# Kernel optimization log

Hardware: AMD Instinct MI355X
Metric: run time of the kernel (lower is better)

## Reference

```python
import jax, jax.numpy as jnp
import numpy as np

H = 8  # num_heads
EPS = 1e-5

def _layernorm(x, g, b):
    mu = jnp.mean(x, axis=-1, keepdims=True)
    var = jnp.var(x, axis=-1, keepdims=True)
    return (x - mu) * jax.lax.rsqrt(var + EPS) * g + b

def setup_inputs() -> dict:
    key = jax.random.key(0)
    ks = jax.random.split(key, 16)
    B, S, D, F = 1, 4096, 512, 2048
    s = 1.0 / np.sqrt(D)
    inp = {
        'x': jax.random.normal(ks[0], (B, S, D), jnp.float32),
        'mask': jax.random.randint(ks[1], (S, S), 0, 2, jnp.int32),
        'wq': jax.random.normal(ks[2], (D, D), jnp.float32) * s,
        'bq': jnp.zeros((D,), jnp.float32),
        'wk': jax.random.normal(ks[3], (D, D), jnp.float32) * s,
        'bk': jnp.zeros((D,), jnp.float32),
        'wv': jax.random.normal(ks[4], (D, D), jnp.float32) * s,
        'bv': jnp.zeros((D,), jnp.float32),
        'wo': jax.random.normal(ks[5], (D, D), jnp.float32) * s,
        'bo': jnp.zeros((D,), jnp.float32),
        'w1': jax.random.normal(ks[6], (D, F), jnp.float32) * s,
        'b1': jnp.zeros((F,), jnp.float32),
        'w2': jax.random.normal(ks[7], (F, D), jnp.float32) * (1.0 / np.sqrt(F)),
        'b2': jnp.zeros((D,), jnp.float32),
        'g1': jnp.ones((D,), jnp.float32),
        'be1': jnp.zeros((D,), jnp.float32),
        'g2': jnp.ones((D,), jnp.float32),
        'be2': jnp.zeros((D,), jnp.float32),
    }
    return inp

def reference(x, mask, wq, bq, wk, bk, wv, bv, wo, bo, w1, b1, w2, b2, g1, be1, g2, be2):
    B, S, D = x.shape
    Dh = D // H

    def split(t):  # (B,S,D) -> (B,H,S,Dh)
        return t.reshape(B, S, H, Dh).transpose(0, 2, 1, 3)

    q = split(x @ wq + bq)
    k = split(x @ wk + bk)
    v = split(x @ wv + bv)

    # naive attention: full (B,H,S,S) scores, NO 1/sqrt(Dh) scaling (faithful to source)
    scores = jnp.einsum('bhsd,bhtd->bhst', q, k)
    scores = jnp.where(mask == 0, jnp.float32(-1e9), scores)
    attn = jax.nn.softmax(scores, axis=-1)
    out = jnp.einsum('bhst,bhtd->bhsd', attn, v)
    out = out.transpose(0, 2, 1, 3).reshape(B, S, D) @ wo + bo

    x = _layernorm(x + out, g1, be1)  # dropout is identity at inference
    ff = jax.nn.relu(x @ w1 + b1) @ w2 + b2
    x = _layernorm(x + ff, g2, be2)
    return x
```

## Files before the change

### kernel.cpp

```cpp
#include <hip/hip_runtime.h>

typedef unsigned short u16;
typedef unsigned int u32;
typedef unsigned long long u64;
typedef __attribute__((ext_vector_type(4))) float f32x4;
typedef __attribute__((ext_vector_type(8))) short bf16x8;
typedef __attribute__((ext_vector_type(4))) u16 u16x4;
typedef __attribute__((ext_vector_type(2))) u32 u32x2;

#define DEV __device__ __forceinline__

DEV u16 f2bf(float f) {
  union { float f; u32 u; } c; c.f = f;
  u32 u = c.u;
  u += 0x7fffu + ((u >> 16) & 1u);
  return (u16)(u >> 16);
}
DEV u32 fbits(float f) { union { float f; u32 u; } c; c.f = f; return c.u; }
DEV u32 packbits(u32 a, u32 b) {
  return __builtin_amdgcn_perm(b, a, 0x07060302u);
}

DEV void gload_lds16(const void* g, void* l) {
  __builtin_amdgcn_global_load_lds(
      (const __attribute__((address_space(1))) u32*)(u64)g,
      (__attribute__((address_space(3))) u32*)(u32)(u64)l,
      16, 0, 0);
}

struct PrepW { const float* w; u16* th; int R, C, gxmask, gxshift; };
struct PrepArgs {
  const float* x; u16* xh;
  const int* mask; unsigned long long* mbits;
  PrepW pw[6];
};

__global__ __launch_bounds__(256) void prep(PrepArgs a) {
  __shared__ float t[32][33];
  int b = blockIdx.x, tid = threadIdx.x;
  if (b < 2048) {
    int i = (b * 256 + tid) * 4;
    f32x4 v = *(const f32x4*)(a.x + i);
    u16x4 h;
#pragma unroll
    for (int j = 0; j < 4; ++j) h[j] = f2bf(v[j]);
    *(u16x4*)(a.xh + i) = h;
    return;
  }
  b -= 2048;
  if (b < 3072) {
    int wi, base;
    if (b < 1024) { wi = b >> 8; base = b & 255; }
    else if (b < 2048) { wi = 4; base = b - 1024; }
    else { wi = 5; base = b - 2048; }
    PrepW p = a.pw[wi];
    int c0 = (base & p.gxmask) * 32, r0 = (base >> p.gxshift) * 32;
    int tx = tid & 31, ty = tid >> 5;
#pragma unroll
    for (int i = 0; i < 4; ++i)
      t[ty + 8 * i][tx] = p.w[(size_t)(r0 + ty + 8 * i) * p.C + c0 + tx];
    __syncthreads();
#pragma unroll
    for (int i = 0; i < 4; ++i)
      p.th[(size_t)(c0 + ty + 8 * i) * p.R + r0 + tx] = f2bf(t[tx][ty + 8 * i]);
    return;
  }
  b -= 3072;
  size_t i = (size_t)b * 256 + tid;
  unsigned long long bb = __ballot(a.mask[i] != 0);
  if ((tid & 63) == 0) a.mbits[i >> 6] = bb;
}

struct QkvArgs {
  const u16* Ah;
  const u16* Bh[3];
  const float* bias[3];
  u16 *Qh, *Kh, *Vt;
};

__global__ __launch_bounds__(256) void gemm_qkv(QkvArgs a) {
  const int K = 512;
  const float L2E = 1.44269504088896340736f;
  const int z = blockIdx.z;
  const u16* __restrict__ Bh = a.Bh[z];
  const float* __restrict__ bias = a.bias[z];
  const int bn = blockIdx.x * 128, bm = blockIdx.y * 128;
  const int tid = threadIdx.x;
  const int wave = tid >> 6, lane = tid & 63;
  const int l16 = lane & 15, quad = lane >> 4;
  const int wm = (wave >> 1) * 64, wn = (wave & 1) * 64;

  __shared__ u16 sA[2][128 * 32];
  __shared__ u16 sB[2][128 * 32];

  const int srow = wave * 32 + (lane >> 2);
  const int scol = (lane & 3) * 8;
  const u16* srcA0 = a.Ah + (size_t)(bm + srow) * K + scol;
  const u16* srcB0 = Bh + (size_t)(bn + srow) * K + scol;
  const size_t half_off = (size_t)16 * K;

  auto prefetchG = [&](int kt, int buf) {
    u16* dA = sA[buf] + wave * 1024;
    u16* dB = sB[buf] + wave * 1024;
    gload_lds16(srcA0 + kt, dA);
    gload_lds16(srcA0 + half_off + kt, dA + 512);
    gload_lds16(srcB0 + kt, dB);
    gload_lds16(srcB0 + half_off + kt, dB + 512);
  };

  f32x4 acc[4][4] = {};
  prefetchG(0, 0);

  for (int i = 0; i < 16; ++i) {
    __syncthreads();
    if (i + 1 < 16) prefetchG((i + 1) << 5, (i + 1) & 1);
    const u16* bufA = sA[i & 1];
    const u16* bufB = sB[i & 1];

    bf16x8 a_h[4], b_h[4];
#pragma unroll
    for (int mt = 0; mt < 4; ++mt)
      a_h[mt] = *(const bf16x8*)(bufA + (wm + mt * 16 + l16) * 32 + quad * 8);
#pragma unroll
    for (int nt = 0; nt < 4; ++nt)
      b_h[nt] = *(const bf16x8*)(bufB + (wn + nt * 16 + l16) * 32 + quad * 8);
#pragma unroll
    for (int mt = 0; mt < 4; ++mt)
#pragma unroll
      for (int nt = 0; nt < 4; ++nt)
        acc[mt][nt] = __builtin_amdgcn_mfma_f32_16x16x32_bf16(a_h[mt], b_h[nt], acc[mt][nt], 0, 0, 0);
  }

  if (z == 2) {
#pragma unroll
    for (int nt = 0; nt < 4; ++nt) {
      int col = bn + wn + nt * 16 + l16;
      float bv = bias[col];
#pragma unroll
      for (int mt = 0; mt < 4; ++mt) {
        int row0 = bm + wm + mt * 16 + quad * 4;
        u16x4 o;
#pragma unroll
        for (int r = 0; r < 4; ++r) o[r] = f2bf(acc[mt][nt][r] + bv);
        *(u16x4*)(a.Vt + (size_t)col * 4096 + row0) = o;
      }
    }
  } else {
    u16* __restrict__ C = (z == 0) ? a.Qh : a.Kh;
    float scale = (z == 0) ? L2E : 1.f;
#pragma unroll
    for (int mt = 0; mt < 4; ++mt)
#pragma unroll
      for (int nt = 0; nt < 4; ++nt) {
        int col = bn + wn + nt * 16 + l16;
        float bv = bias[col];
#pragma unroll
        for (int r = 0; r < 4; ++r) {
          int row = bm + wm + mt * 16 + quad * 4 + r;
          C[(size_t)row * 512 + col] = f2bf((acc[mt][nt][r] + bv) * scale);
        }
      }
  }
}

template <int RELU, int BF16OUT, int NSPLIT>
__global__ __launch_bounds__(256) void gemm_bt(const u16* __restrict__ Ah,
                                               const u16* __restrict__ Bh,
                                               const float* __restrict__ bias,
                                               float* __restrict__ Cf,
                                               float* __restrict__ Cf2,
                                               u16* __restrict__ Ch,
                                               int N, int K) {
  const int z = (NSPLIT > 1) ? blockIdx.z : 0;
  const int Ksub = K / NSPLIT;
  const int kbeg = z * Ksub;
  const int bn = blockIdx.x * 128, bm = blockIdx.y * 128;
  const int tid = threadIdx.x;
  const int wave = tid >> 6, lane = tid & 63;
  const int l16 = lane & 15, quad = lane >> 4;
  const int wm = (wave >> 1) * 64, wn = (wave & 1) * 64;

  __shared__ u16 sA[2][128 * 32];
  __shared__ u16 sB[2][128 * 32];

  const int srow = wave * 32 + (lane >> 2);
  const int scol = (lane & 3) * 8;
  const u16* srcA0 = Ah + (size_t)(bm + srow) * K + kbeg + scol;
  const u16* srcB0 = Bh + (size_t)(bn + srow) * K + kbeg + scol;
  const size_t half_off = (size_t)16 * K;

  auto prefetchG = [&](int kt, int buf) {
    u16* dA = sA[buf] + wave * 1024;
    u16* dB = sB[buf] + wave * 1024;
    gload_lds16(srcA0 + kt, dA);
    gload_lds16(srcA0 + half_off + kt, dA + 512);
    gload_lds16(srcB0 + kt, dB);
    gload_lds16(srcB0 + half_off + kt, dB + 512);
  };

  f32x4 acc[4][4] = {};
  prefetchG(0, 0);

  const int steps = Ksub >> 5;
  for (int i = 0; i < steps; ++i) {
    __syncthreads();
    if (i + 1 < steps) prefetchG((i + 1) << 5, (i + 1) & 1);
    const u16* bufA = sA[i & 1];
    const u16* bufB = sB[i & 1];

    bf16x8 a_h[4], b_h[4];
#pragma unroll
    for (int mt = 0; mt < 4; ++mt)
      a_h[mt] = *(const bf16x8*)(bufA + (wm + mt * 16 + l16) * 32 + quad * 8);
#pragma unroll
    for (int nt = 0; nt < 4; ++nt)
      b_h[nt] = *(const bf16x8*)(bufB + (wn + nt * 16 + l16) * 32 + quad * 8);
#pragma unroll
    for (int mt = 0; mt < 4; ++mt)
#pragma unroll
      for (int nt = 0; nt < 4; ++nt)
        acc[mt][nt] = __builtin_amdgcn_mfma_f32_16x16x32_bf16(a_h[mt], b_h[nt], acc[mt][nt], 0, 0, 0);
  }

  float* __restrict__ Co = (NSPLIT > 1 && z == 1) ? Cf2 : Cf;
#pragma unroll
  for (int mt = 0; mt < 4; ++mt)
#pragma unroll
    for (int nt = 0; nt < 4; ++nt) {
      int col = bn + wn + nt * 16 + l16;
      float bv = (bias && z == 0) ? bias[col] : 0.f;
#pragma unroll
      for (int r = 0; r < 4; ++r) {
        int row = bm + wm + mt * 16 + quad * 4 + r;
        float v = acc[mt][nt][r] + bv;
        if (RELU) v = fmaxf(v, 0.f);
        size_t oidx = (size_t)row * N + col;
        if (BF16OUT) Ch[oidx] = f2bf(v);
        else Co[oidx] = v;
      }
    }
}

struct AttnIO { float* O[4]; float* lp; };

__global__ __launch_bounds__(256) void attn(const u16* __restrict__ Qh,
                                            const u16* __restrict__ Kh,
                                            const u16* __restrict__ Vt,
                                            const u64* __restrict__ mb64,
                                            AttnIO io) {
  const int S = 4096, D = 512;
  const int h = blockIdx.x >> 2, chunk = blockIdx.x & 3;
  const int tid = threadIdx.x, wave = tid >> 6, lane = tid & 63;
  const int l16 = lane & 15, quad = lane >> 4;
  const int q0w = blockIdx.y * 128 + wave * 32;
  const int kbeg = chunk * 1024;
  const int sw = l16 & 7;

  __shared__ u16 sK[64 * 64];
  __shared__ u16 sV[2][80 * 64];
  __shared__ u16 sP[4][32 * 40];
  u16* myP = &sP[wave][0];

  if (tid < 32) ((u64*)(sV[tid >> 4] + 64 * 64))[tid & 15] = 0x3F803F803F803F80ULL;

  const int skey = lane >> 3;
  const int sch  = lane & 7;
  const u16* srcK = Kh + (size_t)(kbeg + wave * 8 + skey) * D + h * 64 + ((sch ^ skey) * 8);
  const u16* srcV = Vt + (size_t)(h * 64 + wave * 8 + skey) * S + kbeg + ((sch ^ skey) * 8);
  u16* dstK = sK + wave * 512;

  auto stageK = [&](int it) {
    const u16* p = srcK + (size_t)it * 64 * D;
    gload_lds16(p, dstK);
    gload_lds16(p + (size_t)32 * D, dstK + 32 * 64);
  };
  auto stageV = [&](int it) {
    const u16* p = srcV + it * 64;
    u16* d = sV[it & 1] + wave * 512;
    gload_lds16(p, d);
    gload_lds16(p + (size_t)32 * S, d + 32 * 64);
  };

  bf16x8 qf[2][2];
#pragma unroll
  for (int qt = 0; qt < 2; ++qt)
#pragma unroll
    for (int kd = 0; kd < 2; ++kd)
      qf[qt][kd] = *(const bf16x8*)(Qh + (size_t)(q0w + qt * 16 + l16) * D + h * 64 + kd * 32 + quad * 8);

  f32x4 accO[2][5] = {};
  const int wbase = kbeg >> 6;

  stageV(0);
  stageK(0);
  u64 wmCur[2];
#pragma unroll
  for (int qt = 0; qt < 2; ++qt)
    wmCur[qt] = mb64[(size_t)(q0w + qt * 16 + l16) * 64 + wbase];

  for (int it = 0; it < 16; ++it) {
    __syncthreads();
    if (it + 1 < 16) stageV(it + 1);
    u64 wmNext[2] = {0, 0};
    if (it + 1 < 16) {
#pragma unroll
      for (int qt = 0; qt < 2; ++qt)
        wmNext[qt] = mb64[(size_t)(q0w + qt * 16 + l16) * 64 + wbase + it + 1];
    }
    u32 wlo[2], whi[2];
#pragma unroll
    for (int qt = 0; qt < 2; ++qt) {
      wlo[qt] = (u32)(wmCur[qt] >> (quad * 4));
      whi[qt] = (u32)(wmCur[qt] >> (quad * 4 + 32));
    }

    f32x4 sc[4][2];
#pragma unroll
    for (int kt4 = 0; kt4 < 4; ++kt4) {
      const u16* arow = sK + (kt4 * 16 + l16) * 64;
      bf16x8 ka0 = *(const bf16x8*)(arow + ((quad ^ sw) * 8));
      bf16x8 ka1 = *(const bf16x8*)(arow + (((4 + quad) ^ sw) * 8));
#pragma unroll
      for (int qt = 0; qt < 2; ++qt) {
        f32x4 s = {};
        s = __builtin_amdgcn_mfma_f32_16x16x32_bf16(ka0, qf[qt][0], s, 0, 0, 0);
        s = __builtin_amdgcn_mfma_f32_16x16x32_bf16(ka1, qf[qt][1], s, 0, 0, 0);
        sc[kt4][qt] = s;
      }
    }
#pragma unroll
    for (int k2 = 0; k2 < 2; ++k2) {
#pragma unroll
      for (int qt = 0; qt < 2; ++qt) {
        u32 pb[4];
#pragma unroll
        for (int r = 0; r < 4; ++r) {
          u32 m = (u32)((int)(wlo[qt] << (31 - (k2 * 16 + r))) >> 31);
          pb[r] = fbits(__builtin_amdgcn_exp2f(sc[k2][qt][r])) & m;
        }
        u32x2 pk = {packbits(pb[0], pb[1]), packbits(pb[2], pb[3])};
        *(u32x2*)(myP + (qt * 16 + l16) * 40 + k2 * 16 + quad * 4) = pk;
      }
    }
    __syncthreads();
    if (it + 1 < 16) stageK(it + 1);
    const u16* bV = sV[it & 1];

    {
      bf16x8 pa[2];
#pragma unroll
      for (int qt = 0; qt < 2; ++qt)
        pa[qt] = *(const bf16x8*)(myP + (qt * 16 + l16) * 40 + quad * 8);
#pragma unroll
      for (int nt = 0; nt < 5; ++nt) {
        bf16x8 vf = *(const bf16x8*)(bV + (nt * 16 + l16) * 64 + ((quad ^ sw) * 8));
#pragma unroll
        for (int qt = 0; qt < 2; ++qt)
          accO[qt][nt] = __builtin_amdgcn_mfma_f32_16x16x32_bf16(pa[qt], vf, accO[qt][nt], 0, 0, 0);
      }
    }
#pragma unroll
    for (int k2 = 0; k2 < 2; ++k2) {
#pragma unroll
      for (int qt = 0; qt < 2; ++qt) {
        u32 pb[4];
#pragma unroll
        for (int r = 0; r < 4; ++r) {
          u32 m = (u32)((int)(whi[qt] << (31 - (k2 * 16 + r))) >> 31);
          pb[r] = fbits(__builtin_amdgcn_exp2f(sc[2 + k2][qt][r])) & m;
        }
        u32x2 pk = {packbits(pb[0], pb[1]), packbits(pb[2], pb[3])};
        *(u32x2*)(myP + (qt * 16 + l16) * 40 + k2 * 16 + quad * 4) = pk;
      }
    }
    {
      bf16x8 pa[2];
#pragma unroll
      for (int qt = 0; qt < 2; ++qt)
        pa[qt] = *(const bf16x8*)(myP + (qt * 16 + l16) * 40 + quad * 8);
#pragma unroll
      for (int nt = 0; nt < 5; ++nt) {
        bf16x8 vf = *(const bf16x8*)(bV + (nt * 16 + l16) * 64 + (((4 + quad) ^ sw) * 8));
#pragma unroll
        for (int qt = 0; qt < 2; ++qt)
          accO[qt][nt] = __builtin_amdgcn_mfma_f32_16x16x32_bf16(pa[qt], vf, accO[qt][nt], 0, 0, 0);
      }
    }
    wmCur[0] = wmNext[0];
    wmCur[1] = wmNext[1];
  }

  float* Op = io.O[chunk];
#pragma unroll
  for (int qt = 0; qt < 2; ++qt)
#pragma unroll
    for (int nt = 0; nt < 4; ++nt)
#pragma unroll
      for (int r = 0; r < 4; ++r) {
        int row = q0w + qt * 16 + quad * 4 + r;
        Op[((size_t)h * S + row) * 64 + nt * 16 + l16] = accO[qt][nt][r];
      }
  if (l16 == 0)
#pragma unroll
    for (int qt = 0; qt < 2; ++qt)
#pragma unroll
      for (int r = 0; r < 4; ++r)
        io.lp[((size_t)h * 4 + chunk) * S + q0w + qt * 16 + quad * 4 + r] = accO[qt][4][r];
}

__global__ __launch_bounds__(256) void attn_combine(AttnIO io, u16* __restrict__ ctx) {
  const int S = 4096;
  int i = (blockIdx.x * 256 + threadIdx.x);
  int row = i >> 7;
  int col4 = (i & 127) * 4;
  int h = col4 >> 6, c = col4 & 63;
  size_t ob = ((size_t)h * S + row) * 64 + c;
  f32x4 o = {0.f, 0.f, 0.f, 0.f};
  float l = 0.f;
#pragma unroll
  for (int p = 0; p < 4; ++p) {
    o += *(const f32x4*)(io.O[p] + ob);
    l += io.lp[((size_t)h * 4 + p) * S + row];
  }
  float rl = 1.f / l;
  u16x4 out;
#pragma unroll
  for (int j = 0; j < 4; ++j) out[j] = f2bf(o[j] * rl);
  *(u16x4*)(ctx + (size_t)row * 512 + col4) = out;
}

__global__ __launch_bounds__(256) void resid_ln(const float* __restrict__ X,
                                                const float* __restrict__ Y,
                                                const float* __restrict__ Y2,
                                                const float* __restrict__ g,
                                                const float* __restrict__ b,
                                                float* __restrict__ outF,
                                                u16* __restrict__ outH) {
  int row = blockIdx.x * 4 + (int)(threadIdx.x >> 6);
  int lane = threadIdx.x & 63;
  const float* x0 = X + (size_t)row * 512;
  const float* y0 = Y + (size_t)row * 512;
  int c0 = lane * 4, c1 = 256 + lane * 4;
  f32x4 v0 = *(const f32x4*)(x0 + c0) + *(const f32x4*)(y0 + c0);
  f32x4 v1 = *(const f32x4*)(x0 + c1) + *(const f32x4*)(y0 + c1);
  if (Y2) {
    const float* y2 = Y2 + (size_t)row * 512;
    v0 += *(const f32x4*)(y2 + c0);
    v1 += *(const f32x4*)(y2 + c1);
  }
  float s = 0.f, s2 = 0.f;
#pragma unroll
  for (int j = 0; j < 4; ++j) {
    s += v0[j] + v1[j];
    s2 += v0[j] * v0[j] + v1[j] * v1[j];
  }
#pragma unroll
  for (int m = 1; m < 64; m <<= 1) {
    s += __shfl_xor(s, m);
    s2 += __shfl_xor(s2, m);
  }
  float mean = s * (1.f / 512.f);
  float var = s2 * (1.f / 512.f) - mean * mean;
  float rs = rsqrtf(var + 1e-5f);
  f32x4 o0, o1;
#pragma unroll
  for (int j = 0; j < 4; ++j) {
    o0[j] = (v0[j] - mean) * rs * g[c0 + j] + b[c0 + j];
    o1[j] = (v1[j] - mean) * rs * g[c1 + j] + b[c1 + j];
  }
  if (outF) {
    *(f32x4*)(outF + (size_t)row * 512 + c0) = o0;
    *(f32x4*)(outF + (size_t)row * 512 + c1) = o1;
  }
  if (outH) {
    u16x4 h0, h1;
#pragma unroll
    for (int j = 0; j < 4; ++j) { h0[j] = f2bf(o0[j]); h1[j] = f2bf(o1[j]); }
    *(u16x4*)(outH + (size_t)row * 512 + c0) = h0;
    *(u16x4*)(outH + (size_t)row * 512 + c1) = h1;
  }
}

extern "C" void kernel_launch(void* const* d_in, const int* in_sizes, int n_in,
                              void* d_out, int out_size, void* d_ws, size_t ws_size,
                              hipStream_t stream) {
  (void)in_sizes; (void)n_in; (void)out_size; (void)ws_size;
  const float* x   = (const float*)d_in[0];
  const int*   mask= (const int*)d_in[1];
  const float* wq  = (const float*)d_in[2];
  const float* bq  = (const float*)d_in[3];
  const float* wk  = (const float*)d_in[4];
  const float* bk  = (const float*)d_in[5];
  const float* wv  = (const float*)d_in[6];
  const float* bv  = (const float*)d_in[7];
  const float* wo  = (const float*)d_in[8];
  const float* bo  = (const float*)d_in[9];
  const float* w1  = (const float*)d_in[10];
  const float* b1  = (const float*)d_in[11];
  const float* w2  = (const float*)d_in[12];
  const float* b2  = (const float*)d_in[13];
  const float* g1  = (const float*)d_in[14];
  const float* be1 = (const float*)d_in[15];
  const float* g2  = (const float*)d_in[16];
  const float* be2 = (const float*)d_in[17];

  const int S = 4096, D = 512, F = 2048;
  char* ws = (char*)d_ws;
  size_t cur = 0;
  auto alloc = [&](size_t bytes) {
    char* p = ws + cur;
    cur += (bytes + 255) & ~(size_t)255;
    return p;
  };
  u16* wqT = (u16*)alloc((size_t)D * D * 2);
  u16* wkT = (u16*)alloc((size_t)D * D * 2);
  u16* wvT = (u16*)alloc((size_t)D * D * 2);
  u16* woT = (u16*)alloc((size_t)D * D * 2);
  u16* w1T = (u16*)alloc((size_t)D * F * 2);
  u16* w2T = (u16*)alloc((size_t)D * F * 2);
  u32* mbits = (u32*)alloc((size_t)S * S / 8);
  u16* xh = (u16*)alloc((size_t)S * D * 2);
  u16* Qh = (u16*)alloc((size_t)S * D * 2);
  u16* Kh = (u16*)alloc((size_t)S * D * 2);
  u16* Vt = (u16*)alloc((size_t)S * D * 2);
  u16* hx = (u16*)alloc((size_t)S * D * 2); (void)hx;
  u16* ctx = (u16*)alloc((size_t)S * D * 2);
  float* x1 = (float*)alloc((size_t)S * D * 4);
  u16* x1h = (u16*)alloc((size_t)S * D * 2);
  float* Opart0 = (float*)alloc((size_t)S * D * 4);
  float* Oex = (float*)alloc((size_t)2 * S * D * 4);
  AttnIO io;
  io.O[0] = Opart0;
  io.O[1] = x1;
  io.O[2] = Oex;
  io.O[3] = Oex + (size_t)S * D;
  io.lp = (float*)x1h;
  float* proj = Opart0;
  float* projB = Oex + (size_t)S * D;
  u16* hbuf = Qh;
  float* ff2 = Oex;
  float* ff2B = Oex + (size_t)S * D;

  PrepArgs pa;
  pa.x = x; pa.xh = xh;
  pa.mask = mask; pa.mbits = (unsigned long long*)mbits;
  pa.pw[0] = {wq, wqT, D, D, 15, 4};
  pa.pw[1] = {wk, wkT, D, D, 15, 4};
  pa.pw[2] = {wv, wvT, D, D, 15, 4};
  pa.pw[3] = {wo, woT, D, D, 15, 4};
  pa.pw[4] = {w1, w1T, D, F, 63, 6};
  pa.pw[5] = {w2, w2T, F, D, 15, 4};

  QkvArgs qa;
  qa.Ah = xh;
  qa.Bh[0] = wqT; qa.Bh[1] = wkT; qa.Bh[2] = wvT;
  qa.bias[0] = bq; qa.bias[1] = bk; qa.bias[2] = bv;
  qa.Qh = Qh; qa.Kh = Kh; qa.Vt = Vt;

  prep<<<70656, 256, 0, stream>>>(pa);
  gemm_qkv<<<dim3(4, 32, 3), 256, 0, stream>>>(qa);
  attn<<<dim3(32, 32), 256, 0, stream>>>(Qh, Kh, Vt, (const u64*)mbits, io);
  attn_combine<<<(S * D / 4) / 256, 256, 0, stream>>>(io, ctx);
  gemm_bt<0, 0, 2><<<dim3(4, 32, 2), 256, 0, stream>>>(ctx, woT, bo, proj, projB, nullptr, D, D);
  resid_ln<<<S / 4, 256, 0, stream>>>(x, proj, projB, g1, be1, x1, x1h);
  gemm_bt<1, 1, 1><<<dim3(16, 32), 256, 0, stream>>>(x1h, w1T, b1, nullptr, nullptr, hbuf, F, D);
  gemm_bt<0, 0, 2><<<dim3(4, 32, 2), 256, 0, stream>>>(hbuf, w2T, b2, ff2, ff2B, nullptr, D, F);
  resid_ln<<<S / 4, 256, 0, stream>>>(x1, ff2, ff2B, g2, be2, (float*)d_out, nullptr);
}
```

Measured before the change: 298.8 us.

## Compute softmax row sums in registers, swizzle P buffer, split-K 4 for output GEMMs

```diff
diff --git a/kernel.cpp b/kernel.cpp
--- a/kernel.cpp
+++ b/kernel.cpp
@@ -17,6 +17,7 @@
   return (u16)(u >> 16);
 }
 DEV u32 fbits(float f) { union { float f; u32 u; } c; c.f = f; return c.u; }
+DEV float bcast(u32 u) { union { u32 u; float f; } c; c.u = u; return c.f; }
 DEV u32 packbits(u32 a, u32 b) {
   return __builtin_amdgcn_perm(b, a, 0x07060302u);
 }
@@ -163,14 +164,13 @@
   }
 }
 
+struct GOut { float* f[4]; u16* h; };
+
 template <int RELU, int BF16OUT, int NSPLIT>
 __global__ __launch_bounds__(256) void gemm_bt(const u16* __restrict__ Ah,
                                                const u16* __restrict__ Bh,
                                                const float* __restrict__ bias,
-                                               float* __restrict__ Cf,
-                                               float* __restrict__ Cf2,
-                                               u16* __restrict__ Ch,
-                                               int N, int K) {
+                                               GOut out, int N, int K) {
   const int z = (NSPLIT > 1) ? blockIdx.z : 0;
   const int Ksub = K / NSPLIT;
   const int kbeg = z * Ksub;
@@ -222,7 +222,7 @@
         acc[mt][nt] = __builtin_amdgcn_mfma_f32_16x16x32_bf16(a_h[mt], b_h[nt], acc[mt][nt], 0, 0, 0);
   }
 
-  float* __restrict__ Co = (NSPLIT > 1 && z == 1) ? Cf2 : Cf;
+  float* __restrict__ Co = out.f[z];
 #pragma unroll
   for (int mt = 0; mt < 4; ++mt)
 #pragma unroll
@@ -235,7 +235,7 @@
         float v = acc[mt][nt][r] + bv;
         if (RELU) v = fmaxf(v, 0.f);
         size_t oidx = (size_t)row * N + col;
-        if (BF16OUT) Ch[oidx] = f2bf(v);
+        if (BF16OUT) out.h[oidx] = f2bf(v);
         else Co[oidx] = v;
       }
     }
@@ -255,13 +255,12 @@
   const int q0w = blockIdx.y * 128 + wave * 32;
   const int kbeg = chunk * 1024;
   const int sw = l16 & 7;
+  const int psw = l16 & 3;
 
   __shared__ u16 sK[64 * 64];
-  __shared__ u16 sV[2][80 * 64];
-  __shared__ u16 sP[4][32 * 40];
+  __shared__ u16 sV[2][64 * 64];
+  __shared__ u16 sP[4][32 * 32];
   u16* myP = &sP[wave][0];
-
-  if (tid < 32) ((u64*)(sV[tid >> 4] + 64 * 64))[tid & 15] = 0x3F803F803F803F80ULL;
 
   const int skey = lane >> 3;
   const int sch  = lane & 7;
@@ -288,7 +287,8 @@
     for (int kd = 0; kd < 2; ++kd)
       qf[qt][kd] = *(const bf16x8*)(Qh + (size_t)(q0w + qt * 16 + l16) * D + h * 64 + kd * 32 + quad * 8);
 
-  f32x4 accO[2][5] = {};
+  f32x4 accO[2][4] = {};
+  float l_lane[2] = {0.f, 0.f};
   const int wbase = kbeg >> 6;
 
   stageV(0);
@@ -338,8 +338,10 @@
           u32 m = (u32)((int)(wlo[qt] << (31 - (k2 * 16 + r))) >> 31);
           pb[r] = fbits(__builtin_amdgcn_exp2f(sc[k2][qt][r])) & m;
         }
+        l_lane[qt] += (bcast(pb[0]) + bcast(pb[1])) + (bcast(pb[2]) + bcast(pb[3]));
         u32x2 pk = {packbits(pb[0], pb[1]), packbits(pb[2], pb[3])};
-        *(u32x2*)(myP + (qt * 16 + l16) * 40 + k2 * 16 + quad * 4) = pk;
+        int g = (k2 * 2 + (quad >> 1)) ^ psw;
+        *(u32x2*)(myP + (qt * 16 + l16) * 32 + g * 8 + (quad & 1) * 4) = pk;
       }
     }
     __syncthreads();
@@ -350,9 +352,9 @@
       bf16x8 pa[2];
 #pragma unroll
       for (int qt = 0; qt < 2; ++qt)
-        pa[qt] = *(const bf16x8*)(myP + (qt * 16 + l16) * 40 + quad * 8);
-#pragma unroll
-      for (int nt = 0; nt < 5; ++nt) {
+        pa[qt] = *(const bf16x8*)(myP + (qt * 16 + l16) * 32 + ((quad ^ psw) * 8));
+#pragma unroll
+      for (int nt = 0; nt < 4; ++nt) {
         bf16x8 vf = *(const bf16x8*)(bV + (nt * 16 + l16) * 64 + ((quad ^ sw) * 8));
 #pragma unroll
         for (int qt = 0; qt < 2; ++qt)
@@ -369,17 +371,19 @@
           u32 m = (u32)((int)(whi[qt] << (31 - (k2 * 16 + r))) >> 31);
           pb[r] = fbits(__builtin_amdgcn_exp2f(sc[2 + k2][qt][r])) & m;
         }
+        l_lane[qt] += (bcast(pb[0]) + bcast(pb[1])) + (bcast(pb[2]) + bcast(pb[3]));
         u32x2 pk = {packbits(pb[0], pb[1]), packbits(pb[2], pb[3])};
-        *(u32x2*)(myP + (qt * 16 + l16) * 40 + k2 * 16 + quad * 4) = pk;
+        int g = (k2 * 2 + (quad >> 1)) ^ psw;
+        *(u32x2*)(myP + (qt * 16 + l16) * 32 + g * 8 + (quad & 1) * 4) = pk;
       }
     }
     {
       bf16x8 pa[2];
 #pragma unroll
       for (int qt = 0; qt < 2; ++qt)
-        pa[qt] = *(const bf16x8*)(myP + (qt * 16 + l16) * 40 + quad * 8);
-#pragma unroll
-      for (int nt = 0; nt < 5; ++nt) {
+        pa[qt] = *(const bf16x8*)(myP + (qt * 16 + l16) * 32 + ((quad ^ psw) * 8));
+#pragma unroll
+      for (int nt = 0; nt < 4; ++nt) {
         bf16x8 vf = *(const bf16x8*)(bV + (nt * 16 + l16) * 64 + (((4 + quad) ^ sw) * 8));
 #pragma unroll
         for (int qt = 0; qt < 2; ++qt)
@@ -390,6 +394,13 @@
     wmCur[1] = wmNext[1];
   }
 
+#pragma unroll
+  for (int qt = 0; qt < 2; ++qt) {
+    float s = l_lane[qt];
+    s += __shfl_xor(s, 16);
+    s += __shfl_xor(s, 32);
+    l_lane[qt] = s;
+  }
   float* Op = io.O[chunk];
 #pragma unroll
   for (int qt = 0; qt < 2; ++qt)
@@ -400,12 +411,10 @@
         int row = q0w + qt * 16 + quad * 4 + r;
         Op[((size_t)h * S + row) * 64 + nt * 16 + l16] = accO[qt][nt][r];
       }
-  if (l16 == 0)
+  if (quad == 0)
 #pragma unroll
     for (int qt = 0; qt < 2; ++qt)
-#pragma unroll
-      for (int r = 0; r < 4; ++r)
-        io.lp[((size_t)h * 4 + chunk) * S + q0w + qt * 16 + quad * 4 + r] = accO[qt][4][r];
+      io.lp[((size_t)h * 4 + chunk) * S + q0w + qt * 16 + l16] = l_lane[qt];
 }
 
 __global__ __launch_bounds__(256) void attn_combine(AttnIO io, u16* __restrict__ ctx) {
@@ -430,24 +439,24 @@
 }
 
 __global__ __launch_bounds__(256) void resid_ln(const float* __restrict__ X,
-                                                const float* __restrict__ Y,
+                                                const float* __restrict__ Y0,
+                                                const float* __restrict__ Y1,
                                                 const float* __restrict__ Y2,
+                                                const float* __restrict__ Y3,
                                                 const float* __restrict__ g,
                                                 const float* __restrict__ b,
                                                 float* __restrict__ outF,
                                                 u16* __restrict__ outH) {
   int row = blockIdx.x * 4 + (int)(threadIdx.x >> 6);
   int lane = threadIdx.x & 63;
-  const float* x0 = X + (size_t)row * 512;
-  const float* y0 = Y + (size_t)row * 512;
+  size_t rb = (size_t)row * 512;
   int c0 = lane * 4, c1 = 256 + lane * 4;
-  f32x4 v0 = *(const f32x4*)(x0 + c0) + *(const f32x4*)(y0 + c0);
-  f32x4 v1 = *(const f32x4*)(x0 + c1) + *(const f32x4*)(y0 + c1);
-  if (Y2) {
-    const float* y2 = Y2 + (size_t)row * 512;
-    v0 += *(const f32x4*)(y2 + c0);
-    v1 += *(const f32x4*)(y2 + c1);
-  }
+  f32x4 v0 = *(const f32x4*)(X + rb + c0) + *(const f32x4*)(Y0 + rb + c0) +
+             *(const f32x4*)(Y1 + rb + c0) + *(const f32x4*)(Y2 + rb + c0) +
+             *(const f32x4*)(Y3 + rb + c0);
+  f32x4 v1 = *(const f32x4*)(X + rb + c1) + *(const f32x4*)(Y0 + rb + c1) +
+             *(const f32x4*)(Y1 + rb + c1) + *(const f32x4*)(Y2 + rb + c1) +
+             *(const f32x4*)(Y3 + rb + c1);
   float s = 0.f, s2 = 0.f;
 #pragma unroll
   for (int j = 0; j < 4; ++j) {
@@ -469,15 +478,15 @@
     o1[j] = (v1[j] - mean) * rs * g[c1 + j] + b[c1 + j];
   }
   if (outF) {
-    *(f32x4*)(outF + (size_t)row * 512 + c0) = o0;
-    *(f32x4*)(outF + (size_t)row * 512 + c1) = o1;
+    *(f32x4*)(outF + rb + c0) = o0;
+    *(f32x4*)(outF + rb + c1) = o1;
   }
   if (outH) {
     u16x4 h0, h1;
 #pragma unroll
     for (int j = 0; j < 4; ++j) { h0[j] = f2bf(o0[j]); h1[j] = f2bf(o1[j]); }
-    *(u16x4*)(outH + (size_t)row * 512 + c0) = h0;
-    *(u16x4*)(outH + (size_t)row * 512 + c1) = h1;
+    *(u16x4*)(outH + rb + c0) = h0;
+    *(u16x4*)(outH + rb + c1) = h1;
   }
 }
 
@@ -528,18 +537,19 @@
   float* x1 = (float*)alloc((size_t)S * D * 4);
   u16* x1h = (u16*)alloc((size_t)S * D * 2);
   float* Opart0 = (float*)alloc((size_t)S * D * 4);
-  float* Oex = (float*)alloc((size_t)2 * S * D * 4);
+  float* Oex0 = (float*)alloc((size_t)S * D * 4);
+  float* Oex1 = (float*)alloc((size_t)S * D * 4);
+  float* Onew = (float*)alloc((size_t)S * D * 4);
   AttnIO io;
   io.O[0] = Opart0;
   io.O[1] = x1;
-  io.O[2] = Oex;
-  io.O[3] = Oex + (size_t)S * D;
+  io.O[2] = Oex0;
+  io.O[3] = Oex1;
   io.lp = (float*)x1h;
-  float* proj = Opart0;
-  float* projB = Oex + (size_t)S * D;
   u16* hbuf = Qh;
-  float* ff2 = Oex;
-  float* ff2B = Oex + (size_t)S * D;
+  GOut opOut = {{Opart0, Oex0, Oex1, Onew}, nullptr};
+  GOut ff1Out = {{nullptr, nullptr, nullptr, nullptr}, hbuf};
+  GOut ff2Out = {{Opart0, Oex0, Oex1, Onew}, nullptr};
 
   PrepArgs pa;
   pa.x = x; pa.xh = xh;
@@ -561,9 +571,9 @@
   gemm_qkv<<<dim3(4, 32, 3), 256, 0, stream>>>(qa);
   attn<<<dim3(32, 32), 256, 0, stream>>>(Qh, Kh, Vt, (const u64*)mbits, io);
   attn_combine<<<(S * D / 4) / 256, 256, 0, stream>>>(io, ctx);
-  gemm_bt<0, 0, 2><<<dim3(4, 32, 2), 256, 0, stream>>>(ctx, woT, bo, proj, projB, nullptr, D, D);
-  resid_ln<<<S / 4, 256, 0, stream>>>(x, proj, projB, g1, be1, x1, x1h);
-  gemm_bt<1, 1, 1><<<dim3(16, 32), 256, 0, stream>>>(x1h, w1T, b1, nullptr, nullptr, hbuf, F, D);
-  gemm_bt<0, 0, 2><<<dim3(4, 32, 2), 256, 0, stream>>>(hbuf, w2T, b2, ff2, ff2B, nullptr, D, F);
-  resid_ln<<<S / 4, 256, 0, stream>>>(x1, ff2, ff2B, g2, be2, (float*)d_out, nullptr);
-}
+  gemm_bt<0, 0, 4><<<dim3(4, 32, 4), 256, 0, stream>>>(ctx, woT, bo, opOut, D, D);
+  resid_ln<<<S / 4, 256, 0, stream>>>(x, Opart0, Oex0, Oex1, Onew, g1, be1, x1, x1h);
+  gemm_bt<1, 1, 1><<<dim3(16, 32), 256, 0, stream>>>(x1h, w1T, b1, ff1Out, F, D);
+  gemm_bt<0, 0, 4><<<dim3(4, 32, 4), 256, 0, stream>>>(hbuf, w2T, b2, ff2Out, D, F);
+  resid_ln<<<S / 4, 256, 0, stream>>>(x1, Opart0, Oex0, Oex1, Onew, g2, be2, (float*)d_out, nullptr);
+}
```

New measurement: 302.9 us. About the same (+1.4%).
